# Performance work log

Hardware: AMD Instinct MI355X
Metric: run time of the kernel (lower is better)

## Reference

```python
import jax, jax.numpy as jnp
import numpy as np
import math

OUT = 7   # output_size
SR = 2    # sampling_ratio


def _roi_align(feat, rois5, scale):
    """torchvision roi_align (aligned=False) for all rois against one FPN level.
    feat: [B,C,H,W], rois5: [N,5] = (batch_idx, x1, y1, x2, y2). Returns [N,C,OUT,OUT]."""
    B, C, H, W = feat.shape
    b = rois5[:, 0].astype(jnp.int32)
    x1 = rois5[:, 1] * scale
    y1 = rois5[:, 2] * scale
    x2 = rois5[:, 3] * scale
    y2 = rois5[:, 4] * scale
    rw = jnp.maximum(x2 - x1, 1.0)
    rh = jnp.maximum(y2 - y1, 1.0)
    gh = OUT * SR  # sampling grid: ph*SR+iy, sample at (g+0.5)*bin/SR from roi start
    gw = OUT * SR
    ys = y1[:, None] + (jnp.arange(gh, dtype=feat.dtype) + 0.5)[None, :] * (rh / gh)[:, None]  # [N,gh]
    xs = x1[:, None] + (jnp.arange(gw, dtype=feat.dtype) + 0.5)[None, :] * (rw / gw)[:, None]  # [N,gw]
    # torchvision bilinear_interpolate: out-of-range (< -1 or > size) -> 0, else clamp
    vy = (ys >= -1.0) & (ys <= H)
    vx = (xs >= -1.0) & (xs <= W)
    y = jnp.clip(ys, 0.0, H - 1)
    x = jnp.clip(xs, 0.0, W - 1)
    y0f = jnp.floor(y)
    x0f = jnp.floor(x)
    y0 = y0f.astype(jnp.int32)
    x0 = x0f.astype(jnp.int32)
    y1i = jnp.minimum(y0 + 1, H - 1)
    x1i = jnp.minimum(x0 + 1, W - 1)
    ly = y - y0f; hy = 1.0 - ly
    lx = x - x0f; hx = 1.0 - lx
    fT = jnp.transpose(feat, (0, 2, 3, 1))  # [B,H,W,C]

    def gather(yi, xi):
        return fT[b[:, None, None], yi[:, :, None], xi[:, None, :]]  # [N,gh,gw,C]

    w00 = (hy[:, :, None] * hx[:, None, :])[..., None]
    w01 = (hy[:, :, None] * lx[:, None, :])[..., None]
    w10 = (ly[:, :, None] * hx[:, None, :])[..., None]
    w11 = (ly[:, :, None] * lx[:, None, :])[..., None]
    val = (gather(y0, x0) * w00 + gather(y0, x1i) * w01
           + gather(y1i, x0) * w10 + gather(y1i, x1i) * w11)
    val = val * (vy[:, :, None] & vx[:, None, :])[..., None].astype(feat.dtype)
    # average SRxSR samples per output bin -> [N,OUT,OUT,C] -> [N,C,OUT,OUT]
    val = val.reshape(val.shape[0], OUT, SR, OUT, SR, C).mean(axis=(2, 4))
    return jnp.transpose(val, (0, 3, 1, 2))


def setup_inputs() -> dict:
    key = jax.random.key(0)
    ks = jax.random.split(key, 6)
    feat0 = jax.random.normal(ks[0], (2, 256, 200, 200), jnp.float32)
    feat1 = jax.random.normal(ks[1], (2, 256, 100, 100), jnp.float32)
    feat2 = jax.random.normal(ks[2], (2, 256, 50, 50), jnp.float32)
    feat3 = jax.random.normal(ks[3], (2, 256, 25, 25), jnp.float32)
    B, N = 2, 512
    xy1 = jax.random.uniform(ks[4], (B, N, 2), jnp.float32, 0.0, 700.0)
    wh = jax.random.uniform(ks[5], (B, N, 2), jnp.float32, 16.0, 320.0)
    xy2 = jnp.minimum(xy1 + wh, 799.0)
    rois = jnp.concatenate([xy1, xy2], axis=-1)  # [B,N,4] = (x1,y1,x2,y2)
    return {"feat0": feat0, "feat1": feat1, "feat2": feat2, "feat3": feat3,
            "rois": rois, "image_h": 800, "image_w": 800}


def reference(feat0, feat1, feat2, feat3, rois, image_h, image_w):
    feats = [feat0, feat1, feat2, feat3]
    B, N = rois.shape[:2]
    # _convert_to_roi_format: prepend batch index column
    bcol = jnp.repeat(jnp.arange(B, dtype=rois.dtype), N)[:, None]
    rois5 = jnp.concatenate([bcol, rois.reshape(-1, 4)], axis=1)  # [B*N,5]
    # _setup_scales / _get_scales: pow-2-rounded ratio of feature H to image H (static)
    scales = [2.0 ** round(math.log2(f.shape[2] / float(image_h))) for f in feats]
    lvl_min = -math.log2(scales[0])   # 2
    lvl_max = -math.log2(scales[-1])  # 5
    # FPN level routing: k = floor(4 + log2(sqrt(area)/224)), clamped
    area = (rois5[:, 4] - rois5[:, 2]) * (rois5[:, 3] - rois5[:, 1])
    k = jnp.floor(4.0 + jnp.log2(jnp.sqrt(area) / 224.0))
    k = jnp.clip(k, lvl_min, lvl_max) - lvl_min  # in {0,1,2,3}
    out = jnp.zeros((B * N, feats[0].shape[1], OUT, OUT), feats[0].dtype)
    for lvl, (f, s) in enumerate(zip(feats, scales)):
        pooled = _roi_align(f, rois5, s)
        out = jnp.where((k == lvl)[:, None, None, None], pooled, out)
    return out
```

## Files before the change

kernel.cpp:

```cpp
#include <hip/hip_runtime.h>

#define OUTS 7
#define SR 2
#define GRIDW 14
#define NS 196
#define NCH 256
#define NROI 1024
#define NBIN 49

#define L0_OFF 0
#define L1_OFF 20480000
#define L2_OFF 25600000
#define L3_OFF 26880000
#define WS_ELEMS 27200000

static __device__ __forceinline__ unsigned short f2bf(float f) {
    unsigned u = __builtin_bit_cast(unsigned, f);
    u += 0x7fffu + ((u >> 16) & 1u);
    return (unsigned short)(u >> 16);
}

static __device__ __forceinline__ float bfhi(unsigned u) {
    return __builtin_bit_cast(float, u & 0xffff0000u);
}
static __device__ __forceinline__ float bflo(unsigned u) {
    return __builtin_bit_cast(float, u << 16);
}

__global__ __launch_bounds__(256) void nchw_to_nhwc_bf16(
    const float* __restrict__ f0, const float* __restrict__ f1,
    const float* __restrict__ f2, const float* __restrict__ f3,
    unsigned short* __restrict__ ws) {
    __shared__ unsigned short tile[256 * 64];
    int bid = blockIdx.x;
    const float* in; unsigned short* outp; int P, ptiles, local;
    if (bid < 1256)      { in = f0; outp = ws + L0_OFF; P = 40000; ptiles = 157; local = bid; }
    else if (bid < 1576) { in = f1; outp = ws + L1_OFF; P = 10000; ptiles = 40;  local = bid - 1256; }
    else if (bid < 1656) { in = f2; outp = ws + L2_OFF; P = 2500;  ptiles = 10;  local = bid - 1576; }
    else                 { in = f3; outp = ws + L3_OFF; P = 625;   ptiles = 3;   local = bid - 1656; }
    int pt = local % ptiles;
    int rest = local / ptiles;
    int q = rest & 3;
    int b  = rest >> 2;
    int p0 = pt * 256;
    int t = threadIdx.x;
    int l = t & 63, w = t >> 6;

    const float* inb = in + (size_t)(b * NCH + q * 64) * P;
    unsigned short* outb = outp + (size_t)b * P * NCH + q * 64;

#pragma unroll
    for (int i = 0; i < 16; ++i) {
        int c = w * 16 + i;
        int pxb = 4 * l;
        const float* src = inb + (size_t)c * P + p0 + pxb;
        float v[4];
        if (p0 + pxb + 3 < P) {
            float4 f = *(const float4*)src;
            v[0] = f.x; v[1] = f.y; v[2] = f.z; v[3] = f.w;
        } else {
#pragma unroll
            for (int k = 0; k < 4; ++k)
                v[k] = (p0 + pxb + k < P) ? src[k] : 0.0f;
        }
#pragma unroll
        for (int k = 0; k < 4; ++k) {
            int px = pxb + k;
            tile[px * 64 + ((c + px) & 63)] = f2bf(v[k]);
        }
    }
    __syncthreads();

    int j = l & 31;
    int h = l >> 5;
#pragma unroll
    for (int it = 0; it < 32; ++it) {
        int px = w * 64 + it * 2 + h;
        int gp = p0 + px;
        if (gp < P) {
            unsigned lo = tile[px * 64 + ((2 * j + px) & 63)];
            unsigned hi = tile[px * 64 + ((2 * j + 1 + px) & 63)];
            *(unsigned*)(outb + (size_t)gp * NCH + 2 * j) = lo | (hi << 16);
        }
    }
}

__global__ __launch_bounds__(256) void roi_gather_nhwc(
    const unsigned short* __restrict__ nhwc,
    const float* __restrict__ rois,
    float* __restrict__ out) {
    __shared__ int   s_off[4][NS];
    __shared__ float s_w[4][NS];
    __shared__ float lds_out[64 * 53];

    int n = blockIdx.x >> 2;
    int q = blockIdx.x & 3;
    int tid = threadIdx.x;
    int b = n >> 9;

    float x1 = rois[n * 4 + 0];
    float y1 = rois[n * 4 + 1];
    float x2 = rois[n * 4 + 2];
    float y2 = rois[n * 4 + 3];
    float area = (y2 - y1) * (x2 - x1);
    float kf = floorf(4.0f + log2f(sqrtf(area) / 224.0f));
    kf = fminf(fmaxf(kf, 2.0f), 5.0f);
    int lvl = (int)kf - 2;
    float scale = ldexpf(0.25f, -lvl);
    int H, W; size_t base;
    switch (lvl) {
        case 0:  H = 200; W = 200; base = L0_OFF; break;
        case 1:  H = 100; W = 100; base = L1_OFF; break;
        case 2:  H = 50;  W = 50;  base = L2_OFF; break;
        default: H = 25;  W = 25;  base = L3_OFF; break;
    }
    float x1s = x1 * scale, y1s = y1 * scale;
    float rw = fmaxf(x2 * scale - x1s, 1.0f);
    float rh = fmaxf(y2 * scale - y1s, 1.0f);
    float sx = rw * (1.0f / GRIDW);
    float sy = rh * (1.0f / GRIDW);

    if (tid < NS) {
        int gy = tid / GRIDW, gx = tid % GRIDW;
        float y = y1s + ((float)gy + 0.5f) * sy;
        float x = x1s + ((float)gx + 0.5f) * sx;
        bool valid = (y >= -1.0f) && (y <= (float)H) && (x >= -1.0f) && (x <= (float)W);
        float yc = fminf(fmaxf(y, 0.0f), (float)(H - 1));
        float xc = fminf(fmaxf(x, 0.0f), (float)(W - 1));
        int y0 = (int)floorf(yc), x0 = (int)floorf(xc);
        int y1i = min(y0 + 1, H - 1), x1i = min(x0 + 1, W - 1);
        float ly = yc - (float)y0, lx = xc - (float)x0;
        float hy = 1.0f - ly, hx = 1.0f - lx;
        float vm = valid ? 1.0f : 0.0f;
        s_off[0][tid] = (y0 * W + x0) * NCH;
        s_off[1][tid] = (y0 * W + x1i) * NCH;
        s_off[2][tid] = (y1i * W + x0) * NCH;
        s_off[3][tid] = (y1i * W + x1i) * NCH;
        s_w[0][tid] = hy * hx * vm;
        s_w[1][tid] = hy * lx * vm;
        s_w[2][tid] = ly * hx * vm;
        s_w[3][tid] = ly * lx * vm;
    }
    __syncthreads();

    int lane = tid & 63;
    int wave = tid >> 6;
    int t = lane >> 4;
    int j = lane & 15;
    const unsigned short* fcq =
        nhwc + base + (size_t)b * (size_t)H * W * NCH + q * 64 + j * 4;

    for (int bin = wave; bin < NBIN; bin += 4) {
        int ph = bin / OUTS, pw = bin - ph * OUTS;
        int sbase = (ph * SR) * GRIDW + pw * SR;
        float4 acc = make_float4(0.f, 0.f, 0.f, 0.f);
#pragma unroll
        for (int k = 0; k < 4; ++k) {
            int s = sbase + (k >> 1) * GRIDW + (k & 1);
            float wgt = s_w[t][s];
            uint2 v = *(const uint2*)(fcq + s_off[t][s]);
            acc.x += wgt * bflo(v.x);
            acc.y += wgt * bfhi(v.x);
            acc.z += wgt * bflo(v.y);
            acc.w += wgt * bfhi(v.y);
        }
        acc.x += __shfl_xor(acc.x, 16, 64);
        acc.y += __shfl_xor(acc.y, 16, 64);
        acc.z += __shfl_xor(acc.z, 16, 64);
        acc.w += __shfl_xor(acc.w, 16, 64);
        acc.x += __shfl_xor(acc.x, 32, 64);
        acc.y += __shfl_xor(acc.y, 32, 64);
        acc.z += __shfl_xor(acc.z, 32, 64);
        acc.w += __shfl_xor(acc.w, 32, 64);
        if (t == 0) {
            lds_out[(4 * j + 0) * 53 + bin] = acc.x * 0.25f;
            lds_out[(4 * j + 1) * 53 + bin] = acc.y * 0.25f;
            lds_out[(4 * j + 2) * 53 + bin] = acc.z * 0.25f;
            lds_out[(4 * j + 3) * 53 + bin] = acc.w * 0.25f;
        }
    }
    __syncthreads();

    float* og = out + (size_t)n * (NCH * NBIN) + (size_t)q * 64 * NBIN;
    for (int i = tid; i < 64 * NBIN; i += 256) {
        int c = i / NBIN;
        int bin = i - c * NBIN;
        og[i] = lds_out[c * 53 + bin];
    }
}


struct RoiMeta {
    float x1, y1, sx, sy;
    int level, b, pad0, pad1;
};

__global__ void prep_rois_kernel(const float* __restrict__ rois,
                                 RoiMeta* __restrict__ meta, int total) {
    int n = blockIdx.x * blockDim.x + threadIdx.x;
    if (n >= total) return;
    float x1 = rois[n * 4 + 0];
    float y1 = rois[n * 4 + 1];
    float x2 = rois[n * 4 + 2];
    float y2 = rois[n * 4 + 3];
    float area = (y2 - y1) * (x2 - x1);
    float k = floorf(4.0f + log2f(sqrtf(area) / 224.0f));
    k = fminf(fmaxf(k, 2.0f), 5.0f);
    int lvl = (int)k - 2;
    float scale = ldexpf(0.25f, -lvl);
    float x1s = x1 * scale;
    float y1s = y1 * scale;
    float rw = fmaxf(x2 * scale - x1s, 1.0f);
    float rh = fmaxf(y2 * scale - y1s, 1.0f);
    RoiMeta m;
    m.x1 = x1s; m.y1 = y1s;
    m.sx = rw / (float)(OUTS * SR);
    m.sy = rh / (float)(OUTS * SR);
    m.level = lvl;
    m.b = n / 512;
    m.pad0 = 0; m.pad1 = 0;
    meta[n] = m;
}

__global__ __launch_bounds__(256) void roi_align_kernel(
    const float* __restrict__ f0, const float* __restrict__ f1,
    const float* __restrict__ f2, const float* __restrict__ f3,
    const RoiMeta* __restrict__ meta, float* __restrict__ out, int total) {
    int idx = blockIdx.x * 256 + threadIdx.x;
    if (idx >= total) return;
    int pw = idx % OUTS;
    int ph = (idx / OUTS) % OUTS;
    int c  = (idx / (OUTS * OUTS)) & (NCH - 1);
    int n  = idx / (OUTS * OUTS * NCH);

    RoiMeta m = meta[n];
    const float* f; int H, W;
    switch (m.level) {
        case 0:  f = f0; H = 200; W = 200; break;
        case 1:  f = f1; H = 100; W = 100; break;
        case 2:  f = f2; H = 50;  W = 50;  break;
        default: f = f3; H = 25;  W = 25;  break;
    }
    const float* fc = f + (size_t)(m.b * NCH + c) * H * W;

    float acc = 0.0f;
#pragma unroll
    for (int iy = 0; iy < SR; ++iy) {
        float y = m.y1 + ((float)(ph * SR + iy) + 0.5f) * m.sy;
        if (y < -1.0f || y > (float)H) continue;
        float yc = fminf(fmaxf(y, 0.0f), (float)(H - 1));
        int y0 = (int)floorf(yc);
        int y1i = min(y0 + 1, H - 1);
        float ly = yc - (float)y0;
        float hy = 1.0f - ly;
        const float* r0 = fc + (size_t)y0 * W;
        const float* r1 = fc + (size_t)y1i * W;
#pragma unroll
        for (int ix = 0; ix < SR; ++ix) {
            float x = m.x1 + ((float)(pw * SR + ix) + 0.5f) * m.sx;
            if (x < -1.0f || x > (float)W) continue;
            float xc = fminf(fmaxf(x, 0.0f), (float)(W - 1));
            int x0 = (int)floorf(xc);
            int x1i = min(x0 + 1, W - 1);
            float lx = xc - (float)x0;
            float hx = 1.0f - lx;
            acc += hy * (hx * r0[x0] + lx * r0[x1i]) +
                   ly * (hx * r1[x0] + lx * r1[x1i]);
        }
    }
    out[idx] = acc * 0.25f;
}


extern "C" void kernel_launch(void* const* d_in, const int* in_sizes, int n_in,
                              void* d_out, int out_size, void* d_ws, size_t ws_size,
                              hipStream_t stream) {
    const float* f0 = (const float*)d_in[0];
    const float* f1 = (const float*)d_in[1];
    const float* f2 = (const float*)d_in[2];
    const float* f3 = (const float*)d_in[3];
    const float* rois = (const float*)d_in[4];
    float* out = (float*)d_out;

    if (ws_size >= (size_t)WS_ELEMS * sizeof(unsigned short)) {
        unsigned short* nhwc = (unsigned short*)d_ws;
        nchw_to_nhwc_bf16<<<1680, 256, 0, stream>>>(f0, f1, f2, f3, nhwc);
        roi_gather_nhwc<<<NROI * 4, 256, 0, stream>>>(nhwc, rois, out);
    } else {
        RoiMeta* meta = (RoiMeta*)d_ws;
        prep_rois_kernel<<<(NROI + 255) / 256, 256, 0, stream>>>(rois, meta, NROI);
        const int total = NROI * NCH * OUTS * OUTS;
        roi_align_kernel<<<(total + 255) / 256, 256, 0, stream>>>(
            f0, f1, f2, f3, meta, out, total);
    }
}
```

Measured before the change: 72.64 us.

## Use direct global-to-LDS loads and smaller tiles in NCHW-to-NHWC transpose

Rewrites the transpose kernel to use 64-pixel tiles staged as fp32 in LDS through global_load_lds (direct global-to-shared DMA), with a fallback path for partial tiles. The grid grows from 1680 to 6656 blocks, and each thread now writes 16-byte packed bf16 stores instead of 4-byte ones. The aim is to cut register round-trips and raise occupancy and store width in the memory-bound layout conversion. The cost is more blocks and possible LDS bank conflicts in the padded fp32 tile reads.

```diff
diff --git a/kernel.cpp b/kernel.cpp
--- a/kernel.cpp
+++ b/kernel.cpp
@@ -27,60 +27,69 @@
     return __builtin_bit_cast(float, u << 16);
 }
 
+typedef const __attribute__((address_space(1))) unsigned int* gas_ptr;
+typedef __attribute__((address_space(3))) unsigned int* las_ptr;
+
 __global__ __launch_bounds__(256) void nchw_to_nhwc_bf16(
     const float* __restrict__ f0, const float* __restrict__ f1,
     const float* __restrict__ f2, const float* __restrict__ f3,
     unsigned short* __restrict__ ws) {
-    __shared__ unsigned short tile[256 * 64];
+    __shared__ __align__(16) float tile[16 * 260];
     int bid = blockIdx.x;
     const float* in; unsigned short* outp; int P, ptiles, local;
-    if (bid < 1256)      { in = f0; outp = ws + L0_OFF; P = 40000; ptiles = 157; local = bid; }
-    else if (bid < 1576) { in = f1; outp = ws + L1_OFF; P = 10000; ptiles = 40;  local = bid - 1256; }
-    else if (bid < 1656) { in = f2; outp = ws + L2_OFF; P = 2500;  ptiles = 10;  local = bid - 1576; }
-    else                 { in = f3; outp = ws + L3_OFF; P = 625;   ptiles = 3;   local = bid - 1656; }
+    if (bid < 5000)      { in = f0; outp = ws + L0_OFF; P = 40000; ptiles = 625; local = bid; }
+    else if (bid < 6256) { in = f1; outp = ws + L1_OFF; P = 10000; ptiles = 157; local = bid - 5000; }
+    else if (bid < 6576) { in = f2; outp = ws + L2_OFF; P = 2500;  ptiles = 40;  local = bid - 6256; }
+    else                 { in = f3; outp = ws + L3_OFF; P = 625;   ptiles = 10;  local = bid - 6576; }
     int pt = local % ptiles;
     int rest = local / ptiles;
     int q = rest & 3;
     int b  = rest >> 2;
-    int p0 = pt * 256;
+    int p0 = pt * 64;
     int t = threadIdx.x;
     int l = t & 63, w = t >> 6;
 
     const float* inb = in + (size_t)(b * NCH + q * 64) * P;
     unsigned short* outb = outp + (size_t)b * P * NCH + q * 64;
 
-#pragma unroll
-    for (int i = 0; i < 16; ++i) {
-        int c = w * 16 + i;
-        int pxb = 4 * l;
-        const float* src = inb + (size_t)c * P + p0 + pxb;
-        float v[4];
-        if (p0 + pxb + 3 < P) {
-            float4 f = *(const float4*)src;
-            v[0] = f.x; v[1] = f.y; v[2] = f.z; v[3] = f.w;
-        } else {
-#pragma unroll
-            for (int k = 0; k < 4; ++k)
-                v[k] = (p0 + pxb + k < P) ? src[k] : 0.0f;
-        }
-#pragma unroll
-        for (int k = 0; k < 4; ++k) {
-            int px = pxb + k;
-            tile[px * 64 + ((c + px) & 63)] = f2bf(v[k]);
+    if (p0 + 64 <= P && (P & 3) == 0) {
+        int cl4 = l >> 4;
+        int pc  = l & 15;
+#pragma unroll
+        for (int ii = 0; ii < 4; ++ii) {
+            int i = w * 4 + ii;
+            int c_local = i * 4 + cl4;
+            const float* g = inb + (size_t)c_local * P + p0 + pc * 4;
+            __builtin_amdgcn_global_load_lds(
+                (gas_ptr)(const void*)g,
+                (las_ptr)(void*)&tile[i * 260], 16, 0, 0);
+        }
+    } else {
+        for (int e = t; e < 64 * 64; e += 256) {
+            int c = e >> 6, p = e & 63;
+            float v = (p0 + p < P) ? inb[(size_t)c * P + p0 + p] : 0.0f;
+            tile[(c >> 2) * 260 + (c & 3) * 64 + (p >> 2) * 4 + (p & 3)] = v;
         }
     }
     __syncthreads();
 
-    int j = l & 31;
-    int h = l >> 5;
-#pragma unroll
-    for (int it = 0; it < 32; ++it) {
-        int px = w * 64 + it * 2 + h;
-        int gp = p0 + px;
+    int j = t & 7;
+    int pl = t >> 3;
+#pragma unroll
+    for (int it = 0; it < 2; ++it) {
+        int p = pl + it * 32;
+        int gp = p0 + p;
         if (gp < P) {
-            unsigned lo = tile[px * 64 + ((2 * j + px) & 63)];
-            unsigned hi = tile[px * 64 + ((2 * j + 1 + px) & 63)];
-            *(unsigned*)(outb + (size_t)gp * NCH + 2 * j) = lo | (hi << 16);
+            unsigned pk[4];
+#pragma unroll
+            for (int m = 0; m < 4; ++m) {
+                int c0 = j * 8 + 2 * m;
+                int c1 = c0 + 1;
+                float a  = tile[(c0 >> 2) * 260 + (c0 & 3) * 64 + (p >> 2) * 4 + (p & 3)];
+                float bq = tile[(c1 >> 2) * 260 + (c1 & 3) * 64 + (p >> 2) * 4 + (p & 3)];
+                pk[m] = (unsigned)f2bf(a) | ((unsigned)f2bf(bq) << 16);
+            }
+            *(uint4*)(outb + (size_t)gp * NCH + j * 8) = make_uint4(pk[0], pk[1], pk[2], pk[3]);
         }
     }
 }
@@ -284,7 +293,7 @@
 
     if (ws_size >= (size_t)WS_ELEMS * sizeof(unsigned short)) {
         unsigned short* nhwc = (unsigned short*)d_ws;
-        nchw_to_nhwc_bf16<<<1680, 256, 0, stream>>>(f0, f1, f2, f3, nhwc);
+        nchw_to_nhwc_bf16<<<6656, 256, 0, stream>>>(f0, f1, f2, f3, nhwc);
         roi_gather_nhwc<<<NROI * 4, 256, 0, stream>>>(nhwc, rois, out);
     } else {
         RoiMeta* meta = (RoiMeta*)d_ws;
```

After: 70.56 us. 1.03x faster.
